# Performance work log

Hardware: AMD Instinct MI355X
Metric: run time of the kernel (lower is better)

The kernel has to match this reference:

```python
import jax, jax.numpy as jnp
import numpy as np

B, C, H, W = 16, 64, 48, 48
D = C * W  # xLSTM embedding dim (== C*H since H==W)
K = 5          # phi='S' kernel size
G_CONV = C // 8  # conv groups = 8
G_NORM = 16      # GroupNorm groups
EPS = 1e-5


def setup_inputs() -> dict:
    key = jax.random.key(0)
    ks = jax.random.split(key, 10)
    s = 0.02
    return {
        'x': jax.random.normal(ks[0], (B, C, H, W), jnp.float32),
        'W1': (jax.random.normal(ks[1], (D, 4 * D), jnp.float32) * s),
        'R1': (jax.random.normal(ks[2], (D, 4 * D), jnp.float32) * s),
        'b1': jnp.zeros((4 * D,), jnp.float32),
        'W2': (jax.random.normal(ks[3], (D, 4 * D), jnp.float32) * s),
        'R2': (jax.random.normal(ks[4], (D, 4 * D), jnp.float32) * s),
        'b2': jnp.zeros((4 * D,), jnp.float32),
        'conv_w': jax.random.normal(ks[5], (C, C // G_CONV, K), jnp.float32) * (1.0 / np.sqrt((C // G_CONV) * K)),
        'gn_gamma': jnp.ones((C,), jnp.float32),
        'gn_beta': jnp.zeros((C,), jnp.float32),
    }


def xlstm_stack(x, Wm, Rm, bm):
    """sLSTM-style xLSTM block (exp gating + stabilizer). x: [B,T,D] -> [B,T,D]."""
    Bsz, T, Dm = x.shape
    pre = jnp.einsum('btd,de->bte', x, Wm) + bm  # input projection for all steps

    def step(carry, p):
        h, c, n, m = carry
        g = p + h @ Rm                      # [B,4D]
        it, ft, zt, ot = jnp.split(g, 4, axis=-1)
        m_new = jnp.maximum(ft + m, it)     # stabilizer
        i = jnp.exp(it - m_new)
        f = jnp.exp(ft + m - m_new)
        c_new = f * c + i * jnp.tanh(zt)
        n_new = f * n + i
        h_new = jax.nn.sigmoid(ot) * c_new / (n_new + 1e-6)
        return (h_new, c_new, n_new, m_new), h_new

    z = jnp.zeros((Bsz, Dm), x.dtype)
    _, ys = jax.lax.scan(step, (z, z, z, z), jnp.swapaxes(pre, 0, 1))
    return jnp.swapaxes(ys, 0, 1)  # [B,T,D]


def conv1d_grouped(x, w):
    pad = K // 2
    return jax.lax.conv_general_dilated(
        x, w, window_strides=(1,), padding=[(pad, pad)],
        feature_group_count=G_CONV, dimension_numbers=('NCH', 'OIH', 'NCH'))


def group_norm(x, gamma, beta):
    b, c, L = x.shape
    xg = x.reshape(b, G_NORM, -1)
    mu = xg.mean(-1, keepdims=True)
    var = xg.var(-1, keepdims=True)
    xn = ((xg - mu) * jax.lax.rsqrt(var + EPS)).reshape(b, c, L)
    return xn * gamma[None, :, None] + beta[None, :, None]


def ela_forward(x, W1, R1, b1, W2, R2, b2, conv_w, gn_gamma, gn_beta):
    b, c, h, w = x.shape
    # stack cfg2: sequence over h, features c*w
    y2 = xlstm_stack(x.reshape(b, h, c * w), W2, R2, b2).reshape(b, c, w, h)
    # stack cfg1: sequence over w, features c*h
    y1 = xlstm_stack(x.reshape(b, w, c * h), W1, R1, b1).reshape(b, c, w, h)
    x_h = jnp.mean(y2, axis=3).reshape(b, c, h)
    x_w = jnp.mean(y1, axis=2).reshape(b, c, w)
    x_h = jax.nn.sigmoid(group_norm(conv1d_grouped(x_h, conv_w), gn_gamma, gn_beta)).reshape(b, c, h, 1)
    x_w = jax.nn.sigmoid(group_norm(conv1d_grouped(x_w, conv_w), gn_gamma, gn_beta)).reshape(b, c, 1, w)
    return x_h * x_w * x


def reference(x, W1, R1, b1, W2, R2, b2, conv_w, gn_gamma, gn_beta):
    return ela_forward(x, W1, R1, b1, W2, R2, b2, conv_w, gn_gamma, gn_beta)
```

## Files before the change

kernel.cpp:

```cpp
#include <hip/hip_runtime.h>
#include <hip/hip_bf16.h>


typedef float  f32x4 __attribute__((ext_vector_type(4)));
typedef __bf16 v8bf  __attribute__((ext_vector_type(8)));
typedef __bf16 v4bf  __attribute__((ext_vector_type(4)));

#define MFMA16(a, b, c) __builtin_amdgcn_mfma_f32_16x16x32_bf16((a), (b), (c), 0, 0, 0)

static constexpr size_t OFF_PREP = 0;
static constexpr size_t SZ_PREP  = 37748736;
static constexpr size_t OFF_H0   = 37748736;
static constexpr size_t OFF_H1   = 37945344;
static constexpr size_t OFF_C    = 38141952;
static constexpr size_t OFF_N    = 38535168;
static constexpr size_t OFF_M    = 38928384;
static constexpr size_t OFF_YS   = 39321600;
static constexpr size_t OFF_GATE = 39714816;
static constexpr size_t BASE_END = 40108032;
static constexpr size_t SZ_RPACK = 75497472;
static constexpr size_t OFF_RA   = BASE_END;
static constexpr size_t OFF_RB   = BASE_END + SZ_RPACK;
static constexpr size_t END_A    = OFF_RB + SZ_RPACK;

__device__ __forceinline__ void gl_lds16(const void* g, void* l) {
    __builtin_amdgcn_global_load_lds(
        (const __attribute__((address_space(1))) unsigned int*)g,
        (__attribute__((address_space(3))) unsigned int*)l, 16, 0, 0);
}

__global__ __launch_bounds__(256) void zero_kernel(f32x4* __restrict__ p, int n) {
    int i = blockIdx.x * 256 + threadIdx.x;
    if (i < n) { f32x4 z = 0.0f; p[i] = z; }
}

__global__ __launch_bounds__(256) void pack_x_kernel(const float* __restrict__ x,
                                                     __bf16* __restrict__ dst) {
    int gi = blockIdx.x * 256 + threadIdx.x;
    int lane = gi & 63;
    int rest = gi >> 6;
    int sub = rest & 7; rest >>= 3;
    int kc = rest % 96, mb = rest / 96;
    int r = mb * 128 + sub * 16 + (lane & 15);
    int t = r >> 4, b = r & 15;
    int k = kc * 32 + (lane >> 4) * 8;
    const f32x4* s = (const f32x4*)(x + (size_t)b * 147456 + (size_t)t * 3072 + k);
    f32x4 v0 = s[0], v1 = s[1];
    v8bf o;
#pragma unroll
    for (int j = 0; j < 4; ++j) { o[j] = (__bf16)v0[j]; o[4 + j] = (__bf16)v1[j]; }
    ((v8bf*)dst)[gi] = o;
}

__global__ __launch_bounds__(256) void pack_B_kernel(const float* __restrict__ src0,
                                                     const float* __restrict__ src1,
                                                     __bf16* __restrict__ dst0,
                                                     __bf16* __restrict__ dst1) {
    int nb = blockIdx.x, kc = blockIdx.y, m = blockIdx.z;
    const float* src = m ? src1 : src0;
    __bf16* dst = m ? dst1 : dst0;
    int tid = threadIdx.x;
    __shared__ float tile[32][133];
    int kr = tid >> 3, nc0 = (tid & 7) * 16;
    const f32x4* s4 = (const f32x4*)(src + (size_t)(kc * 32 + kr) * 12288 + nb * 128 + nc0);
    f32x4 v0 = s4[0], v1 = s4[1], v2 = s4[2], v3 = s4[3];
#pragma unroll
    for (int r = 0; r < 4; ++r) {
        tile[kr][nc0 + r]      = v0[r];
        tile[kr][nc0 + 4 + r]  = v1[r];
        tile[kr][nc0 + 8 + r]  = v2[r];
        tile[kr][nc0 + 12 + r] = v3[r];
    }
    __syncthreads();
    __bf16* db = dst + (size_t)(nb * 96 + kc) * 4096;
#pragma unroll
    for (int c = 0; c < 2; ++c) {
        int lidx = tid * 2 + c;
        int sub = lidx >> 6, lane = lidx & 63;
        int kb = (lane >> 4) * 8, nn = sub * 16 + (lane & 15);
        v8bf o;
#pragma unroll
        for (int j = 0; j < 8; ++j) o[j] = (__bf16)tile[kb + j][nn];
        ((v8bf*)db)[lidx] = o;
    }
}

__global__ __launch_bounds__(256) void pack_R_kernel(const float* __restrict__ src0,
                                                     const float* __restrict__ src1,
                                                     __bf16* __restrict__ dst0,
                                                     __bf16* __restrict__ dst1) {
    int nb = blockIdx.x, kc = blockIdx.y, m = blockIdx.z;
    const float* src = m ? src1 : src0;
    __bf16* dst = m ? dst1 : dst0;
    int tid = threadIdx.x;
    __shared__ float tile[32][133];
    int kr = tid >> 3, nc0 = (tid & 7) * 16;
    const f32x4* s4 = (const f32x4*)(src + (size_t)(kc * 32 + kr) * 12288 + nb * 128 + nc0);
    f32x4 v0 = s4[0], v1 = s4[1], v2 = s4[2], v3 = s4[3];
#pragma unroll
    for (int r = 0; r < 4; ++r) {
        tile[kr][nc0 + r]      = v0[r];
        tile[kr][nc0 + 4 + r]  = v1[r];
        tile[kr][nc0 + 8 + r]  = v2[r];
        tile[kr][nc0 + 12 + r] = v3[r];
    }
    __syncthreads();
#pragma unroll
    for (int c = 0; c < 2; ++c) {
        int lidx = tid * 2 + c;
        int sub = lidx >> 6, lane = lidx & 63;
        int kb = (lane >> 4) * 8, nn = sub * 16 + (lane & 15);
        v8bf o;
#pragma unroll
        for (int j = 0; j < 8; ++j) o[j] = (__bf16)tile[kb + j][nn];
        int ct = nb * 8 + sub;
        int nt = ct % 192, fi = ct / 192;
        size_t off = (((size_t)nt * 96 + kc) * 4 + fi) * 64 + lane;
        ((v8bf*)dst)[off] = o;
    }
}

__global__ __launch_bounds__(256) void pre_gemm_packed(const __bf16* __restrict__ Apack,
                                                       const __bf16* __restrict__ Bp0,
                                                       const __bf16* __restrict__ Bp1,
                                                       __bf16* __restrict__ preP) {
    int nb = blockIdx.x, mb = blockIdx.y, stack = blockIdx.z;
    const char* Bpack = (const char*)(stack ? Bp1 : Bp0);
    int tid = threadIdx.x, wave = tid >> 6, lane = tid & 63;
    __shared__ alignas(16) __bf16 As[4096];
    __shared__ alignas(16) __bf16 Bs[4096];
    f32x4 acc[4][4];
#pragma unroll
    for (int i = 0; i < 4; ++i)
#pragma unroll
        for (int j = 0; j < 4; ++j) acc[i][j] = 0.0f;

    for (int kc = 0; kc < 96; ++kc) {
        size_t atile = (size_t)(mb * 96 + kc) * 8192;
        size_t btile = (size_t)(nb * 96 + kc) * 8192;
        int chunk = wave * 2048;
        gl_lds16((const char*)Apack + atile + chunk + lane * 16,        (char*)As + chunk);
        gl_lds16((const char*)Apack + atile + chunk + 1024 + lane * 16, (char*)As + chunk + 1024);
        gl_lds16(Bpack + btile + chunk + lane * 16,        (char*)Bs + chunk);
        gl_lds16(Bpack + btile + chunk + 1024 + lane * 16, (char*)Bs + chunk + 1024);
        __syncthreads();
        const v8bf* A8 = (const v8bf*)As;
        const v8bf* B8 = (const v8bf*)Bs;
        v8bf a[4], b[4];
#pragma unroll
        for (int mi = 0; mi < 4; ++mi) a[mi] = A8[((wave >> 1) * 4 + mi) * 64 + lane];
#pragma unroll
        for (int ni = 0; ni < 4; ++ni) b[ni] = B8[((wave & 1) * 4 + ni) * 64 + lane];
#pragma unroll
        for (int mi = 0; mi < 4; ++mi)
#pragma unroll
            for (int ni = 0; ni < 4; ++ni) acc[mi][ni] = MFMA16(a[mi], b[ni], acc[mi][ni]);
        __syncthreads();
    }
#pragma unroll
    for (int mi = 0; mi < 4; ++mi)
#pragma unroll
        for (int ni = 0; ni < 4; ++ni) {
            int mt = mb * 8 + (wave >> 1) * 4 + mi;
            int nt4 = nb * 8 + (wave & 1) * 4 + ni;
            v4bf o;
#pragma unroll
            for (int r = 0; r < 4; ++r) o[r] = (__bf16)acc[mi][ni][r];
            ((v4bf*)preP)[(((size_t)stack * 48 + mt) * 768 + nt4) * 64 + lane] = o;
        }
}

__global__ __launch_bounds__(256) void pre_gemm(const __bf16* __restrict__ Apack,
                                                const float* __restrict__ W1,
                                                const float* __restrict__ W2,
                                                __bf16* __restrict__ preP) {
    int nb = blockIdx.x, mb = blockIdx.y, stack = blockIdx.z;
    const float* W = stack ? W2 : W1;
    int tid = threadIdx.x, wave = tid >> 6, lane = tid & 63;
    __shared__ alignas(16) __bf16 As[4096];
    __shared__ alignas(16) __bf16 Bs[4096];
    __shared__ float tile[32][133];
    f32x4 acc[4][4];
#pragma unroll
    for (int i = 0; i < 4; ++i)
#pragma unroll
        for (int j = 0; j < 4; ++j) acc[i][j] = 0.0f;

    int kr = tid >> 3, nc0 = (tid & 7) * 16;
    for (int kc = 0; kc < 96; ++kc) {
        size_t atile = (size_t)(mb * 96 + kc) * 8192;
        int chunk = wave * 2048;
        gl_lds16((const char*)Apack + atile + chunk + lane * 16,        (char*)As + chunk);
        gl_lds16((const char*)Apack + atile + chunk + 1024 + lane * 16, (char*)As + chunk + 1024);
        const f32x4* s4 = (const f32x4*)(W + (size_t)(kc * 32 + kr) * 12288 + nb * 128 + nc0);
        f32x4 v0 = s4[0], v1 = s4[1], v2 = s4[2], v3 = s4[3];
#pragma unroll
        for (int r = 0; r < 4; ++r) {
            tile[kr][nc0 + r]      = v0[r];
            tile[kr][nc0 + 4 + r]  = v1[r];
            tile[kr][nc0 + 8 + r]  = v2[r];
            tile[kr][nc0 + 12 + r] = v3[r];
        }
        __syncthreads();
#pragma unroll
        for (int c = 0; c < 2; ++c) {
            int lidx = tid * 2 + c;
            int sub = lidx >> 6, l2 = lidx & 63;
            int kb = (l2 >> 4) * 8, nn = sub * 16 + (l2 & 15);
            v8bf o;
#pragma unroll
            for (int j = 0; j < 8; ++j) o[j] = (__bf16)tile[kb + j][nn];
            ((v8bf*)Bs)[lidx] = o;
        }
        __syncthreads();
        const v8bf* A8 = (const v8bf*)As;
        const v8bf* B8 = (const v8bf*)Bs;
        v8bf a[4], b[4];
#pragma unroll
        for (int mi = 0; mi < 4; ++mi) a[mi] = A8[((wave >> 1) * 4 + mi) * 64 + lane];
#pragma unroll
        for (int ni = 0; ni < 4; ++ni) b[ni] = B8[((wave & 1) * 4 + ni) * 64 + lane];
#pragma unroll
        for (int mi = 0; mi < 4; ++mi)
#pragma unroll
            for (int ni = 0; ni < 4; ++ni) acc[mi][ni] = MFMA16(a[mi], b[ni], acc[mi][ni]);
        __syncthreads();
    }
#pragma unroll
    for (int mi = 0; mi < 4; ++mi)
#pragma unroll
        for (int ni = 0; ni < 4; ++ni) {
            int mt = mb * 8 + (wave >> 1) * 4 + mi;
            int nt4 = nb * 8 + (wave & 1) * 4 + ni;
            v4bf o;
#pragma unroll
            for (int r = 0; r < 4; ++r) o[r] = (__bf16)acc[mi][ni][r];
            ((v4bf*)preP)[(((size_t)stack * 48 + mt) * 768 + nt4) * 64 + lane] = o;
        }
}

__global__ __launch_bounds__(512) void step_kernel(
    const __bf16* __restrict__ Rp0, const __bf16* __restrict__ Rp1,
    const __bf16* __restrict__ hread, __bf16* __restrict__ hwrite,
    const __bf16* __restrict__ preP,
    const float* __restrict__ bias1, const float* __restrict__ bias2,
    float* __restrict__ cbuf, float* __restrict__ nbuf, float* __restrict__ mbuf,
    float* __restrict__ ysum, int t) {
    int nt = blockIdx.x, stack = blockIdx.y;
    int tid = threadIdx.x, wave = tid >> 6, lane = tid & 63;
    const v8bf* Rp = (const v8bf*)(stack ? Rp1 : Rp0);
    const v8bf* hA = (const v8bf*)hread + (size_t)stack * 96 * 64;
    size_t base0 = (size_t)nt * 24576 + lane;
    int kcs = wave * 12;
    f32x4 acc[4];
#pragma unroll
    for (int i = 0; i < 4; ++i) acc[i] = 0.0f;

    v8bf a0 = hA[(size_t)kcs * 64 + lane];
    v8bf bf[4];
#pragma unroll
    for (int i = 0; i < 4; ++i) bf[i] = Rp[base0 + (size_t)kcs * 256 + i * 64];
    for (int kk = 0; kk < 12; ++kk) {
        v8bf a1 = a0;
        v8bf bn[4];
        if (kk < 11) {
            int kc1 = kcs + kk + 1;
            a1 = hA[(size_t)kc1 * 64 + lane];
#pragma unroll
            for (int i = 0; i < 4; ++i) bn[i] = Rp[base0 + (size_t)kc1 * 256 + i * 64];
        } else {
#pragma unroll
            for (int i = 0; i < 4; ++i) bn[i] = bf[i];
        }
#pragma unroll
        for (int i = 0; i < 4; ++i) acc[i] = MFMA16(a0, bf[i], acc[i]);
        a0 = a1;
#pragma unroll
        for (int i = 0; i < 4; ++i) bf[i] = bn[i];
    }

    __shared__ f32x4 red4[8][4][64];
#pragma unroll
    for (int i = 0; i < 4; ++i) red4[wave][i][lane] = acc[i];
    __syncthreads();

    if (wave == 0) {
        const float* bias = stack ? bias2 : bias1;
        f32x4 g[4];
#pragma unroll
        for (int i = 0; i < 4; ++i) {
            f32x4 s = red4[0][i][lane];
#pragma unroll
            for (int w = 1; w < 8; ++w) s += red4[w][i][lane];
            g[i] = s;
        }
        int fcol = nt * 16 + (lane & 15);
        int bq = (lane >> 4) * 4;
#pragma unroll
        for (int i = 0; i < 4; ++i) {
            v4bf pv = ((const v4bf*)preP)[(((size_t)stack * 48 + t) * 768 + (i * 192 + nt)) * 64 + lane];
            float bv = bias[i * 3072 + fcol];
#pragma unroll
            for (int r = 0; r < 4; ++r) g[i][r] += (float)pv[r] + bv;
        }
        size_t sidx = ((size_t)stack * 192 + nt) * 64 + lane;
        f32x4 cc = ((f32x4*)cbuf)[sidx];
        f32x4 nn = ((f32x4*)nbuf)[sidx];
        f32x4 mm = ((f32x4*)mbuf)[sidx];
        int kc = fcol >> 5, ko = fcol & 31;
        __bf16* hw = hwrite + ((size_t)stack * 96 + kc) * 512 + (size_t)(ko >> 3) * 128 + (ko & 7);
        int flat = t * 3072 + fcol;
        int cch = flat / 2304;
        int rem = flat - cch * 2304;
        int u = rem / 48;
        int v = rem - u * 48;
        int yidx = cch * 48 + (stack ? u : v);
        float* yb = ysum + (size_t)stack * 16 * 3072;
#pragma unroll
        for (int r = 0; r < 4; ++r) {
            int brow = bq + r;
            float it = g[0][r], ft = g[1][r], zt = g[2][r], ot = g[3][r];
            float mnew = fmaxf(ft + mm[r], it);
            float iv = __expf(it - mnew);
            float fv = __expf(ft + mm[r] - mnew);
            float cnew = fv * cc[r] + iv * tanhf(zt);
            float nnew = fv * nn[r] + iv;
            float sg = 1.0f / (1.0f + __expf(-ot));
            float h = sg * cnew / (nnew + 1e-6f);
            cc[r] = cnew; nn[r] = nnew; mm[r] = mnew;
            hw[(size_t)brow * 8] = (__bf16)h;
            atomicAdd(yb + (size_t)brow * 3072 + yidx, h);
        }
        ((f32x4*)cbuf)[sidx] = cc;
        ((f32x4*)nbuf)[sidx] = nn;
        ((f32x4*)mbuf)[sidx] = mm;
    }
}

__global__ __launch_bounds__(256) void conv_gn_kernel(const float* __restrict__ ysum,
                                                      const float* __restrict__ cw,
                                                      const float* __restrict__ gamma,
                                                      const float* __restrict__ beta,
                                                      float* __restrict__ gatebuf) {
    int bi = blockIdx.x;
    int s = bi >> 4, b = bi & 15;
    int tid = threadIdx.x;
    __shared__ float in0[3072], cvout[3072], cws[2560];
    __shared__ float r1[16][16], r2[16][16], mu_s[16], rs_s[16];
    const float* src = ysum + (size_t)(s * 16 + b) * 3072;
    for (int e = tid; e < 3072; e += 256) in0[e] = src[e] * (1.0f / 48.0f);
    for (int e = tid; e < 2560; e += 256) cws[e] = cw[e];
    __syncthreads();
    for (int e = tid; e < 3072; e += 256) {
        int co = e / 48, p = e - co * 48;
        int g = co >> 3;
        const float* wrow = cws + co * 40;
        const float* irow = in0 + g * 8 * 48;
        float a = 0.f;
#pragma unroll
        for (int ci = 0; ci < 8; ++ci)
#pragma unroll
            for (int q = 0; q < 5; ++q) {
                int pp = p + q - 2;
                if (pp >= 0 && pp < 48) a += wrow[ci * 5 + q] * irow[ci * 48 + pp];
            }
        cvout[e] = a;
    }
    __syncthreads();
    int gn = tid >> 4, ln = tid & 15;
    float s1 = 0.f, s2 = 0.f;
    for (int ii = ln; ii < 192; ii += 16) {
        float v = cvout[gn * 192 + ii];
        s1 += v; s2 += v * v;
    }
    r1[gn][ln] = s1; r2[gn][ln] = s2;
    __syncthreads();
    if (tid < 16) {
        float a = 0.f, c2 = 0.f;
        for (int ii = 0; ii < 16; ++ii) { a += r1[tid][ii]; c2 += r2[tid][ii]; }
        float mu = a * (1.0f / 192.0f);
        float var = c2 * (1.0f / 192.0f) - mu * mu;
        mu_s[tid] = mu;
        rs_s[tid] = rsqrtf(var + 1e-5f);
    }
    __syncthreads();
    float* dst = gatebuf + (size_t)(s * 16 + b) * 3072;
    for (int e = tid; e < 3072; e += 256) {
        int c = e / 48;
        int gg = c >> 2;
        float xn = (cvout[e] - mu_s[gg]) * rs_s[gg] * gamma[c] + beta[c];
        dst[e] = 1.0f / (1.0f + __expf(-xn));
    }
}

__global__ __launch_bounds__(256) void final_kernel(const float* __restrict__ x,
                                                    const float* __restrict__ gatebuf,
                                                    float* __restrict__ out) {
    int gid = blockIdx.x * 256 + threadIdx.x;
    int wi4 = gid % 12;
    int rest = gid / 12;
    int hi = rest % 48;
    int bc = rest / 48;
    int b = bc >> 6, c = bc & 63;
    f32x4 xv = ((const f32x4*)x)[gid];
    float gh = gatebuf[(size_t)(16 + b) * 3072 + c * 48 + hi];
    f32x4 gw = *(const f32x4*)(gatebuf + (size_t)b * 3072 + c * 48 + wi4 * 4);
    f32x4 o;
#pragma unroll
    for (int k = 0; k < 4; ++k) o[k] = xv[k] * gh * gw[k];
    ((f32x4*)out)[gid] = o;
}

extern "C" void kernel_launch(void* const* d_in, const int* in_sizes, int n_in,
                              void* d_out, int out_size, void* d_ws, size_t ws_size,
                              hipStream_t stream) {
    const float* x     = (const float*)d_in[0];
    const float* W1    = (const float*)d_in[1];
    const float* R1    = (const float*)d_in[2];
    const float* b1    = (const float*)d_in[3];
    const float* W2    = (const float*)d_in[4];
    const float* R2    = (const float*)d_in[5];
    const float* b2    = (const float*)d_in[6];
    const float* cw    = (const float*)d_in[7];
    const float* gamma = (const float*)d_in[8];
    const float* beta  = (const float*)d_in[9];

    char* ws = (char*)d_ws;
    __bf16* seqA = (__bf16*)d_out;
    __bf16* preP = (__bf16*)(ws + OFF_PREP);
    __bf16* h0   = (__bf16*)(ws + OFF_H0);
    __bf16* h1   = (__bf16*)(ws + OFF_H1);
    float* cbuf  = (float*)(ws + OFF_C);
    float* nbuf  = (float*)(ws + OFF_N);
    float* mbuf  = (float*)(ws + OFF_M);
    float* ysum  = (float*)(ws + OFF_YS);
    float* gate  = (float*)(ws + OFF_GATE);

    bool big_ws = ws_size >= END_A;
    __bf16* PA = (__bf16*)(ws + OFF_RA);
    __bf16* PB = (__bf16*)(ws + OFF_RB);

    pack_x_kernel<<<1152, 256, 0, stream>>>(x, seqA);
    if (big_ws) {
        pack_B_kernel<<<dim3(96, 96, 2), 256, 0, stream>>>(W1, W2, PA, PB);
        pre_gemm_packed<<<dim3(96, 6, 2), 256, 0, stream>>>(seqA, PA, PB, preP);
        pack_R_kernel<<<dim3(96, 96, 2), 256, 0, stream>>>(R1, R2, PA, PB);
    } else {
        pre_gemm<<<dim3(96, 6, 2), 256, 0, stream>>>(seqA, W1, W2, preP);
        pack_R_kernel<<<dim3(96, 96, 2), 256, 0, stream>>>(R1, R2, PA, PB);
    }
    zero_kernel<<<480, 256, 0, stream>>>((f32x4*)(ws + OFF_H0), 122880);
    for (int t = 0; t < 48; ++t) {
        const __bf16* hr = (t & 1) ? h1 : h0;
        __bf16* hw       = (t & 1) ? h0 : h1;
        step_kernel<<<dim3(192, 2), 512, 0, stream>>>(PA, PB, hr, hw, preP, b1, b2,
                                                      cbuf, nbuf, mbuf, ysum, t);
    }
    conv_gn_kernel<<<32, 256, 0, stream>>>(ysum, cw, gamma, beta, gate);
    final_kernel<<<2304, 256, 0, stream>>>(x, gate, (float*)d_out);
}
```

Measured before the change: 2.666 ms.

## Replace per-timestep launches with a cooperative persistent kernel and grid barrier

The 48 separate step_kernel launches become a single cooperative persistent kernel of 192 blocks. Each block handles both stacks with four waves apiece, keeps the c/n/m state in registers, and caches part of its recurrent weight slice in registers. Timesteps are separated by an atomic-counter grid barrier, and h is exchanged through system-scope atomic loads and stores. The aim is to remove launch overhead and state round-trips to memory, at the cost of barrier spin latency, a bail-out guard that could break ordering, and higher register pressure. The fallback step_kernel also loses its manual software prefetch in favour of an unrolled loop.

Result: slower. 3.398 ms (+27.5%).

```diff
diff --git a/kernel.cpp b/kernel.cpp
--- a/kernel.cpp
+++ b/kernel.cpp
@@ -239,6 +239,128 @@
         }
 }
 
+__global__ __launch_bounds__(512, 2) void persistent_step(
+    const __bf16* __restrict__ Rp0, const __bf16* __restrict__ Rp1,
+    __bf16* __restrict__ h0, __bf16* __restrict__ h1,
+    const __bf16* __restrict__ preP,
+    const float* __restrict__ bias1, const float* __restrict__ bias2,
+    float* __restrict__ ysum, unsigned* __restrict__ bar) {
+    int nt = blockIdx.x;
+    int tid = threadIdx.x, wave = tid >> 6, lane = tid & 63;
+    int s  = wave >> 2;
+    int wv = wave & 3;
+    const v8bf* Rp = (const v8bf*)(s ? Rp1 : Rp0);
+    size_t base0 = (size_t)nt * 24576 + lane;
+    int kcs = wv * 24;
+    const float* bias = s ? bias2 : bias1;
+    int fcol = nt * 16 + (lane & 15);
+    int bq = (lane >> 4) * 4;
+    int kc2 = fcol >> 5, ko = fcol & 31;
+    float* yb = ysum + (size_t)s * 16 * 3072;
+
+    v8bf rS[8][4];
+#pragma unroll
+    for (int j = 0; j < 8; ++j)
+#pragma unroll
+        for (int i = 0; i < 4; ++i)
+            rS[j][i] = Rp[base0 + (size_t)(kcs + 16 + j) * 256 + i * 64];
+
+    f32x4 cc = 0.0f, nn = 0.0f, mm = 0.0f;
+    const __bf16* hr = h0;
+    __bf16* hwp = h1;
+
+    __shared__ f32x4 red[2][4][4][64];
+
+    for (int t = 0; t < 48; ++t) {
+        const unsigned long long* hq = (const unsigned long long*)hr + (size_t)s * 12288;
+        f32x4 acc[4];
+#pragma unroll
+        for (int i = 0; i < 4; ++i) acc[i] = 0.0f;
+#pragma unroll
+        for (int kk = 0; kk < 24; ++kk) {
+            int kc = kcs + kk;
+            size_t qi = ((size_t)kc * 64 + lane) * 2;
+            unsigned long long q0 = __hip_atomic_load(hq + qi,     __ATOMIC_RELAXED,
+                                                      __HIP_MEMORY_SCOPE_SYSTEM);
+            unsigned long long q1 = __hip_atomic_load(hq + qi + 1, __ATOMIC_RELAXED,
+                                                      __HIP_MEMORY_SCOPE_SYSTEM);
+            unsigned long long tmp[2] = {q0, q1};
+            v8bf a; __builtin_memcpy(&a, tmp, 16);
+            if (kk < 16) {
+#pragma unroll
+                for (int i = 0; i < 4; ++i) {
+                    v8bf b = Rp[base0 + (size_t)kc * 256 + i * 64];
+                    acc[i] = MFMA16(a, b, acc[i]);
+                }
+            } else {
+#pragma unroll
+                for (int i = 0; i < 4; ++i)
+                    acc[i] = MFMA16(a, rS[kk - 16][i], acc[i]);
+            }
+        }
+#pragma unroll
+        for (int i = 0; i < 4; ++i) red[s][wv][i][lane] = acc[i];
+        __syncthreads();
+
+        if (wv == 0) {
+            f32x4 g[4];
+#pragma unroll
+            for (int i = 0; i < 4; ++i) {
+                f32x4 sum = red[s][0][i][lane];
+#pragma unroll
+                for (int w = 1; w < 4; ++w) sum += red[s][w][i][lane];
+                g[i] = sum;
+            }
+#pragma unroll
+            for (int i = 0; i < 4; ++i) {
+                v4bf pv = ((const v4bf*)preP)[(((size_t)s * 48 + t) * 768 + (i * 192 + nt)) * 64 + lane];
+                float bv = bias[i * 3072 + fcol];
+#pragma unroll
+                for (int r = 0; r < 4; ++r) g[i][r] += (float)pv[r] + bv;
+            }
+            __bf16* hwB = hwp + ((size_t)s * 96 + kc2) * 512 + (size_t)(ko >> 3) * 128 + (ko & 7);
+            int flat = t * 3072 + fcol;
+            int cch = flat / 2304;
+            int rem = flat - cch * 2304;
+            int uu = rem / 48;
+            int vv = rem - uu * 48;
+            int yidx = cch * 48 + (s ? uu : vv);
+#pragma unroll
+            for (int r = 0; r < 4; ++r) {
+                int brow = bq + r;
+                float it = g[0][r], ft = g[1][r], zt = g[2][r], ot = g[3][r];
+                float mnew = fmaxf(ft + mm[r], it);
+                float iv = __expf(it - mnew);
+                float fv = __expf(ft + mm[r] - mnew);
+                float cnew = fv * cc[r] + iv * tanhf(zt);
+                float nnew = fv * nn[r] + iv;
+                float sg = 1.0f / (1.0f + __expf(-ot));
+                float h = sg * cnew / (nnew + 1e-6f);
+                cc[r] = cnew; nn[r] = nnew; mm[r] = mnew;
+                __bf16 hb = (__bf16)h;
+                unsigned short hs; __builtin_memcpy(&hs, &hb, 2);
+                __hip_atomic_store((unsigned short*)(hwB + (size_t)brow * 8), hs,
+                                   __ATOMIC_RELAXED, __HIP_MEMORY_SCOPE_SYSTEM);
+                atomicAdd(yb + (size_t)brow * 3072 + yidx, h);
+            }
+        }
+
+        __syncthreads();
+        if (tid == 0) {
+            __hip_atomic_fetch_add(bar, 1u, __ATOMIC_RELAXED, __HIP_MEMORY_SCOPE_SYSTEM);
+            unsigned tgt = (unsigned)(t + 1) * 192u;
+            int guard = 0;
+            while (__hip_atomic_load(bar, __ATOMIC_RELAXED, __HIP_MEMORY_SCOPE_SYSTEM) < tgt) {
+                __builtin_amdgcn_s_sleep(2);
+                if (++guard > 50000) break;
+            }
+        }
+        __syncthreads();
+
+        const __bf16* tmp = hr; hr = hwp; hwp = (__bf16*)tmp;
+    }
+}
+
 __global__ __launch_bounds__(512) void step_kernel(
     const __bf16* __restrict__ Rp0, const __bf16* __restrict__ Rp1,
     const __bf16* __restrict__ hread, __bf16* __restrict__ hwrite,
@@ -255,28 +377,15 @@
     f32x4 acc[4];
 #pragma unroll
     for (int i = 0; i < 4; ++i) acc[i] = 0.0f;
-
-    v8bf a0 = hA[(size_t)kcs * 64 + lane];
-    v8bf bf[4];
-#pragma unroll
-    for (int i = 0; i < 4; ++i) bf[i] = Rp[base0 + (size_t)kcs * 256 + i * 64];
+#pragma unroll 4
     for (int kk = 0; kk < 12; ++kk) {
-        v8bf a1 = a0;
-        v8bf bn[4];
-        if (kk < 11) {
-            int kc1 = kcs + kk + 1;
-            a1 = hA[(size_t)kc1 * 64 + lane];
-#pragma unroll
-            for (int i = 0; i < 4; ++i) bn[i] = Rp[base0 + (size_t)kc1 * 256 + i * 64];
-        } else {
-#pragma unroll
-            for (int i = 0; i < 4; ++i) bn[i] = bf[i];
-        }
-#pragma unroll
-        for (int i = 0; i < 4; ++i) acc[i] = MFMA16(a0, bf[i], acc[i]);
-        a0 = a1;
-#pragma unroll
-        for (int i = 0; i < 4; ++i) bf[i] = bn[i];
+        int kc = kcs + kk;
+        v8bf a = hA[(size_t)kc * 64 + lane];
+        v8bf bb[4];
+#pragma unroll
+        for (int i = 0; i < 4; ++i) bb[i] = Rp[base0 + (size_t)kc * 256 + i * 64];
+#pragma unroll
+        for (int i = 0; i < 4; ++i) acc[i] = MFMA16(a, bb[i], acc[i]);
     }
 
     __shared__ f32x4 red4[8][4][64];
@@ -312,9 +421,9 @@
         int flat = t * 3072 + fcol;
         int cch = flat / 2304;
         int rem = flat - cch * 2304;
-        int u = rem / 48;
-        int v = rem - u * 48;
-        int yidx = cch * 48 + (stack ? u : v);
+        int uu = rem / 48;
+        int vv = rem - uu * 48;
+        int yidx = cch * 48 + (stack ? uu : vv);
         float* yb = ysum + (size_t)stack * 16 * 3072;
 #pragma unroll
         for (int r = 0; r < 4; ++r) {
@@ -435,6 +544,7 @@
     float* mbuf  = (float*)(ws + OFF_M);
     float* ysum  = (float*)(ws + OFF_YS);
     float* gate  = (float*)(ws + OFF_GATE);
+    unsigned* bar = (unsigned*)(ws + OFF_GATE);
 
     bool big_ws = ws_size >= END_A;
     __bf16* PA = (__bf16*)(ws + OFF_RA);
@@ -449,13 +559,29 @@
         pre_gemm<<<dim3(96, 6, 2), 256, 0, stream>>>(seqA, W1, W2, preP);
         pack_R_kernel<<<dim3(96, 96, 2), 256, 0, stream>>>(R1, R2, PA, PB);
     }
-    zero_kernel<<<480, 256, 0, stream>>>((f32x4*)(ws + OFF_H0), 122880);
-    for (int t = 0; t < 48; ++t) {
-        const __bf16* hr = (t & 1) ? h1 : h0;
-        __bf16* hw       = (t & 1) ? h0 : h1;
-        step_kernel<<<dim3(192, 2), 512, 0, stream>>>(PA, PB, hr, hw, preP, b1, b2,
-                                                      cbuf, nbuf, mbuf, ysum, t);
-    }
+    zero_kernel<<<481, 256, 0, stream>>>((f32x4*)(ws + OFF_H0), 122881);
+
+    {
+        const __bf16* a0 = PA; const __bf16* a1 = PB;
+        __bf16* ph0 = h0; __bf16* ph1 = h1;
+        const __bf16* pp = preP;
+        const float* pb1 = b1; const float* pb2 = b2;
+        float* pys = ysum; unsigned* pbar = bar;
+        void* args[] = { (void*)&a0, (void*)&a1, (void*)&ph0, (void*)&ph1,
+                         (void*)&pp, (void*)&pb1, (void*)&pb2, (void*)&pys, (void*)&pbar };
+        hipError_t err = hipLaunchCooperativeKernel(
+            reinterpret_cast<void*>(persistent_step), dim3(192), dim3(512),
+            args, 0, stream);
+        if (err != hipSuccess) {
+            for (int t = 0; t < 48; ++t) {
+                const __bf16* hr = (t & 1) ? h1 : h0;
+                __bf16* hw       = (t & 1) ? h0 : h1;
+                step_kernel<<<dim3(192, 2), 512, 0, stream>>>(PA, PB, hr, hw, preP, b1, b2,
+                                                              cbuf, nbuf, mbuf, ysum, t);
+            }
+        }
+    }
+
     conv_gn_kernel<<<32, 256, 0, stream>>>(ysum, cw, gamma, beta, gate);
     final_kernel<<<2304, 256, 0, stream>>>(x, gate, (float*)d_out);
 }
```

## Split recurrent step K-reduction across paired blocks with flag handoff

Applied to the files above, without the earlier changes.

Each step's R-matmul reduction is now split across two 256-thread blocks instead of one 512-thread block, giving 768 blocks. The second half writes its partial gates to a scratch buffer and raises a per-unit flag. The first half spin-waits on that flag, adds the partials and runs the gate update. This aims to spread the R loads over more CUs, at the cost of inter-block spin-waiting, a risk of deadlock if the pair is not co-resident, and reuse of the output and gate regions as scratch.

After: 3.090 ms. +15.9%, slower.

```diff
diff --git a/kernel.cpp b/kernel.cpp
--- a/kernel.cpp
+++ b/kernel.cpp
@@ -239,19 +239,22 @@
         }
 }
 
-__global__ __launch_bounds__(512) void step_kernel(
+__global__ __launch_bounds__(256) void step_kernel(
     const __bf16* __restrict__ Rp0, const __bf16* __restrict__ Rp1,
     const __bf16* __restrict__ hread, __bf16* __restrict__ hwrite,
     const __bf16* __restrict__ preP,
     const float* __restrict__ bias1, const float* __restrict__ bias2,
     float* __restrict__ cbuf, float* __restrict__ nbuf, float* __restrict__ mbuf,
-    float* __restrict__ ysum, int t) {
-    int nt = blockIdx.x, stack = blockIdx.y;
+    float* __restrict__ ysum, float* __restrict__ Gbuf, unsigned* __restrict__ flags,
+    int t) {
+    int bid = blockIdx.x;
+    int unit = bid >> 1, half = bid & 1;
+    int nt = unit % 192, stack = unit / 192;
     int tid = threadIdx.x, wave = tid >> 6, lane = tid & 63;
     const v8bf* Rp = (const v8bf*)(stack ? Rp1 : Rp0);
     const v8bf* hA = (const v8bf*)hread + (size_t)stack * 96 * 64;
     size_t base0 = (size_t)nt * 24576 + lane;
-    int kcs = wave * 12;
+    int kcs = half * 48 + wave * 12;
     f32x4 acc[4];
 #pragma unroll
     for (int i = 0; i < 4; ++i) acc[i] = 0.0f;
@@ -279,21 +282,52 @@
         for (int i = 0; i < 4; ++i) bf[i] = bn[i];
     }
 
-    __shared__ f32x4 red4[8][4][64];
+    __shared__ f32x4 red4[4][4][64];
 #pragma unroll
     for (int i = 0; i < 4; ++i) red4[wave][i][lane] = acc[i];
     __syncthreads();
 
     if (wave == 0) {
-        const float* bias = stack ? bias2 : bias1;
         f32x4 g[4];
 #pragma unroll
         for (int i = 0; i < 4; ++i) {
             f32x4 s = red4[0][i][lane];
 #pragma unroll
-            for (int w = 1; w < 8; ++w) s += red4[w][i][lane];
+            for (int w = 1; w < 4; ++w) s += red4[w][i][lane];
             g[i] = s;
         }
+        if (half == 1) {
+#pragma unroll
+            for (int i = 0; i < 4; ++i)
+#pragma unroll
+                for (int r = 0; r < 4; ++r)
+                    __hip_atomic_store(
+                        Gbuf + ((((size_t)unit * 4 + i) * 64 + lane) * 4 + r), g[i][r],
+                        __ATOMIC_RELAXED, __HIP_MEMORY_SCOPE_SYSTEM);
+            if (lane == 0)
+                __hip_atomic_fetch_add(flags + unit, 1u, __ATOMIC_RELEASE,
+                                       __HIP_MEMORY_SCOPE_SYSTEM);
+            return;
+        }
+        {
+            unsigned tgt = (unsigned)(t + 1);
+            int guard = 0;
+            while (__hip_atomic_load(flags + unit, __ATOMIC_RELAXED,
+                                     __HIP_MEMORY_SCOPE_SYSTEM) < tgt) {
+                __builtin_amdgcn_s_sleep(2);
+                if (++guard > 10000000) break;
+            }
+            asm volatile("" ::: "memory");
+        }
+#pragma unroll
+        for (int i = 0; i < 4; ++i)
+#pragma unroll
+            for (int r = 0; r < 4; ++r)
+                g[i][r] += __hip_atomic_load(
+                    Gbuf + ((((size_t)unit * 4 + i) * 64 + lane) * 4 + r),
+                    __ATOMIC_RELAXED, __HIP_MEMORY_SCOPE_SYSTEM);
+
+        const float* bias = stack ? bias2 : bias1;
         int fcol = nt * 16 + (lane & 15);
         int bq = (lane >> 4) * 4;
 #pragma unroll
@@ -435,6 +469,8 @@
     float* mbuf  = (float*)(ws + OFF_M);
     float* ysum  = (float*)(ws + OFF_YS);
     float* gate  = (float*)(ws + OFF_GATE);
+    unsigned* flags = (unsigned*)(ws + OFF_GATE);
+    float* gbuf  = (float*)d_out;
 
     bool big_ws = ws_size >= END_A;
     __bf16* PA = (__bf16*)(ws + OFF_RA);
@@ -449,12 +485,13 @@
         pre_gemm<<<dim3(96, 6, 2), 256, 0, stream>>>(seqA, W1, W2, preP);
         pack_R_kernel<<<dim3(96, 96, 2), 256, 0, stream>>>(R1, R2, PA, PB);
     }
-    zero_kernel<<<480, 256, 0, stream>>>((f32x4*)(ws + OFF_H0), 122880);
+    zero_kernel<<<481, 256, 0, stream>>>((f32x4*)(ws + OFF_H0), 122976);
+
     for (int t = 0; t < 48; ++t) {
         const __bf16* hr = (t & 1) ? h1 : h0;
         __bf16* hw       = (t & 1) ? h0 : h1;
-        step_kernel<<<dim3(192, 2), 512, 0, stream>>>(PA, PB, hr, hw, preP, b1, b2,
-                                                      cbuf, nbuf, mbuf, ysum, t);
+        step_kernel<<<768, 256, 0, stream>>>(PA, PB, hr, hw, preP, b1, b2,
+                                             cbuf, nbuf, mbuf, ysum, gbuf, flags, t);
     }
     conv_gn_kernel<<<32, 256, 0, stream>>>(ysum, cw, gamma, beta, gate);
     final_kernel<<<2304, 256, 0, stream>>>(x, gate, (float*)d_out);
```
